# Performance work log

Hardware: AMD Instinct MI355X
Metric: run time of the kernel (lower is better)

## Reference

```python
import jax, jax.numpy as jnp
import numpy as np

E = 1024   # embed_dim
H = 16     # num_heads
DH = E // H
FF = 4096  # intermediate_size
EPS = 1e-5


def layernorm(x, g, b):
    mu = jnp.mean(x, axis=-1, keepdims=True)
    var = jnp.var(x, axis=-1, keepdims=True)
    return (x - mu) * jax.lax.rsqrt(var + EPS) * g + b


def setup_inputs() -> dict:
    key = jax.random.key(0)
    ks = jax.random.split(key, 16)
    s = 0.02
    return {
        "x": jax.random.normal(ks[0], (2, 2048, E), dtype=jnp.float32),
        "ln1_g": jnp.ones((E,), jnp.float32),
        "ln1_b": jnp.zeros((E,), jnp.float32),
        "ln2_g": jnp.ones((E,), jnp.float32),
        "ln2_b": jnp.zeros((E,), jnp.float32),
        # per-head Q/K/V projections stacked: [H, E, DH]
        "wq": jax.random.normal(ks[1], (H, E, DH), jnp.float32) * s,
        "bq": jnp.zeros((H, DH), jnp.float32),
        "wk": jax.random.normal(ks[2], (H, E, DH), jnp.float32) * s,
        "bk": jnp.zeros((H, DH), jnp.float32),
        "wv": jax.random.normal(ks[3], (H, E, DH), jnp.float32) * s,
        "bv": jnp.zeros((H, DH), jnp.float32),
        "wo": jax.random.normal(ks[4], (E, E), jnp.float32) * s,
        "bo": jnp.zeros((E,), jnp.float32),
        "w1": jax.random.normal(ks[5], (E, FF), jnp.float32) * s,
        "b1": jnp.zeros((FF,), jnp.float32),
        "w2": jax.random.normal(ks[6], (FF, E), jnp.float32) * s,
        "b2": jnp.zeros((E,), jnp.float32),
    }


def reference(x, ln1_g, ln1_b, ln2_g, ln2_b, wq, bq, wk, bk, wv, bv,
              wo, bo, w1, b1, w2, b2):
    # --- multi-head attention (pre-LN) ---
    h = layernorm(x, ln1_g, ln1_b)                       # [B,S,E]
    q = jnp.einsum('bse,hed->bhsd', h, wq) + bq[:, None, :]
    k = jnp.einsum('bse,hed->bhsd', h, wk) + bk[:, None, :]
    v = jnp.einsum('bse,hed->bhsd', h, wv) + bv[:, None, :]
    scores = jnp.einsum('bhsd,bhtd->bhst', q, k) / jnp.sqrt(
        jnp.asarray(DH, x.dtype))                        # [B,H,S,S]
    w = jax.nn.softmax(scores, axis=-1)
    attn = jnp.einsum('bhst,bhtd->bhsd', w, v)           # [B,H,S,DH]
    B, _, S, _ = attn.shape
    concat = attn.transpose(0, 2, 1, 3).reshape(B, S, E)  # head concat order
    x = x + concat @ wo + bo
    # --- feed-forward (pre-LN), exact GELU, dropout_p=0 ---
    h2 = layernorm(x, ln2_g, ln2_b)
    ff = jax.nn.gelu(h2 @ w1 + b1, approximate=False) @ w2 + b2
    return x + ff
```

## Files before the change

kernel.cpp:

```cpp
#include <hip/hip_runtime.h>
#include <hip/hip_bf16.h>
#include <math.h>

typedef __attribute__((ext_vector_type(8))) short short8;
typedef __attribute__((ext_vector_type(4))) float f32x4;
typedef __attribute__((ext_vector_type(16))) float f32x16;
typedef __attribute__((ext_vector_type(4))) unsigned u32x4;

#define MFMA_BF16(a, b, c) __builtin_amdgcn_mfma_f32_16x16x32_bf16(a, b, c, 0, 0, 0)
#define MFMA32_BF16(a, b, c) __builtin_amdgcn_mfma_f32_32x32x16_bf16(a, b, c, 0, 0, 0)
#define BAR() __builtin_amdgcn_s_barrier()

#define GLD_LDS16(g, l)                                              \
  __builtin_amdgcn_global_load_lds(                                  \
      (const __attribute__((address_space(1))) void*)(g),            \
      (__attribute__((address_space(3))) void*)(l), 16, 0, 0)

template <int N>
__device__ __forceinline__ void waitcnt_vm() {
  if constexpr (N == 0) asm volatile("s_waitcnt vmcnt(0)" ::: "memory");
  else if constexpr (N == 2) asm volatile("s_waitcnt vmcnt(2)" ::: "memory");
  else if constexpr (N == 4) asm volatile("s_waitcnt vmcnt(4)" ::: "memory");
  else if constexpr (N == 6) asm volatile("s_waitcnt vmcnt(6)" ::: "memory");
  else if constexpr (N == 8) asm volatile("s_waitcnt vmcnt(8)" ::: "memory");
}

__device__ __forceinline__ unsigned cvt_pk_bf16(float lo, float hi) {
  unsigned r;
  asm("v_cvt_pk_bf16_f32 %0, %1, %2" : "=v"(r) : "v"(lo), "v"(hi));
  return r;
}
#define PSWAP(a, b) asm volatile("v_permlane32_swap_b32 %0, %1" : "+v"(a), "+v"(b))

__device__ __forceinline__ unsigned short f2bf(float f) {
  union { float f; unsigned u; } v; v.f = f;
  unsigned r = v.u + 0x7FFFu + ((v.u >> 16) & 1u);
  return (unsigned short)(r >> 16);
}
__device__ __forceinline__ float bf2f(unsigned short u) {
  union { unsigned u; float f; } v; v.u = ((unsigned)u) << 16;
  return v.f;
}

__global__ __launch_bounds__(256) void transpose_cast(
    const float* __restrict__ in, unsigned short* __restrict__ out,
    int R, int C, size_t in_bs, size_t out_bs) {
  __shared__ float t[32][33];
  const float* inp = in + blockIdx.z * in_bs;
  unsigned short* outp = out + blockIdx.z * out_bs;
  const int c0 = blockIdx.x * 32, r0 = blockIdx.y * 32;
  const int tx = threadIdx.x, ty = threadIdx.y;
#pragma unroll
  for (int i = 0; i < 32; i += 8)
    t[ty + i][tx] = inp[(size_t)(r0 + ty + i) * C + c0 + tx];
  __syncthreads();
#pragma unroll
  for (int i = 0; i < 32; i += 8)
    outp[(size_t)(c0 + ty + i) * R + r0 + tx] = f2bf(t[tx][ty + i]);
}

__global__ void concat_bias(const float* __restrict__ bq, const float* __restrict__ bk,
                            const float* __restrict__ bv, float* __restrict__ bcat) {
  int i = blockIdx.x * 256 + threadIdx.x;
  if (i < 1024) bcat[i] = bq[i];
  else if (i < 2048) bcat[i] = bk[i - 1024];
  else if (i < 3072) bcat[i] = bv[i - 2048];
}

__global__ __launch_bounds__(512) void vtrans(
    const unsigned short* __restrict__ qkv, unsigned short* __restrict__ vt) {
  __shared__ unsigned short t[64][65];
  const int bh = blockIdx.y;
  const int s0 = blockIdx.x * 64;
  const int tx = threadIdx.x;
  const int ty = threadIdx.y;
  const unsigned short* in =
      qkv + (size_t)(bh >> 4) * 2048 * 3072 + 2048 + (bh & 15) * 64;
#pragma unroll
  for (int i = 0; i < 8; ++i)
    t[ty * 8 + i][tx] = in[(size_t)(s0 + ty * 8 + i) * 3072 + tx];
  __syncthreads();
  unsigned short* o = vt + (size_t)bh * 64 * 2048 + s0;
#pragma unroll
  for (int i = 0; i < 8; ++i)
    o[(size_t)(ty * 8 + i) * 2048 + tx] = t[tx][ty * 8 + i];
}

__global__ __launch_bounds__(256) void ln_kernel(
    const float* __restrict__ x, const float* __restrict__ g,
    const float* __restrict__ bb, unsigned short* __restrict__ out) {
  const int row = blockIdx.x, tid = threadIdx.x;
  const float4 v = ((const float4*)(x + (size_t)row * 1024))[tid];
  float s = v.x + v.y + v.z + v.w;
  float ss = v.x * v.x + v.y * v.y + v.z * v.z + v.w * v.w;
#pragma unroll
  for (int k = 1; k < 64; k <<= 1) {
    s += __shfl_xor(s, k, 64);
    ss += __shfl_xor(ss, k, 64);
  }
  __shared__ float red[8];
  const int wid = tid >> 6;
  if ((tid & 63) == 0) { red[wid] = s; red[wid + 4] = ss; }
  __syncthreads();
  s = red[0] + red[1] + red[2] + red[3];
  ss = red[4] + red[5] + red[6] + red[7];
  const float mu = s * (1.0f / 1024.0f);
  const float var = ss * (1.0f / 1024.0f) - mu * mu;
  const float rs = rsqrtf(var + 1e-5f);
  const float4 gv = ((const float4*)g)[tid];
  const float4 bv = ((const float4*)bb)[tid];
  ushort4 o;
  o.x = f2bf((v.x - mu) * rs * gv.x + bv.x);
  o.y = f2bf((v.y - mu) * rs * gv.y + bv.y);
  o.z = f2bf((v.z - mu) * rs * gv.z + bv.z);
  o.w = f2bf((v.w - mu) * rs * gv.w + bv.w);
  ((ushort4*)(out + (size_t)row * 1024))[tid] = o;
}

template <int QM, int QN>
__device__ __forceinline__ void mfq(f32x4 (&acc)[8][4], short8 (&af)[4][2],
                                    short8 (&bf)[2][2]) {
  __builtin_amdgcn_s_setprio(1);
#pragma unroll
  for (int i = 0; i < 4; ++i)
#pragma unroll
    for (int nf = 0; nf < 2; ++nf) {
      acc[QM * 4 + i][QN * 2 + nf] =
          MFMA_BF16(af[i][0], bf[nf][0], acc[QM * 4 + i][QN * 2 + nf]);
      acc[QM * 4 + i][QN * 2 + nf] =
          MFMA_BF16(af[i][1], bf[nf][1], acc[QM * 4 + i][QN * 2 + nf]);
    }
  __builtin_amdgcn_s_setprio(0);
}

template <int EPI>
__global__ __launch_bounds__(512, 2) void gemm256(
    const unsigned short* __restrict__ A, const unsigned short* __restrict__ Bt,
    const float* __restrict__ bias, void* __restrict__ Cout,
    int M, int N, int K,
    unsigned short* __restrict__ p0, unsigned short* __restrict__ p1,
    unsigned short* __restrict__ p2, unsigned short* __restrict__ p3) {
  extern __shared__ unsigned short L[];
  const int tid = threadIdx.x;
  const int wv = tid >> 6, lane = tid & 63;
  const int li = lane & 15, gi = lane >> 4;
  const int wm = wv >> 2, wn = wv & 3;
  const int bm = blockIdx.y, bn = blockIdx.x;
  const size_t Ksz = (size_t)K;
  const int KTloc = (K / (int)gridDim.z) >> 6;
  const int k0 = blockIdx.z * (KTloc << 6);

  auto lds = [&](int buf, int op, int half) -> unsigned short* {
    return L + (size_t)(((buf * 2 + op) * 2 + half)) * 8192;
  };

  const int sr8 = tid >> 3;
  const int segG = (tid & 7) ^ (sr8 & 7);
  const unsigned short* Ag = A + (size_t)(bm * 256 + sr8) * Ksz + segG * 8 + k0;
  const unsigned short* Bg = Bt + (size_t)(bn * 256 + sr8) * Ksz + segG * 8 + k0;
  const int wbase = wv * 512;

  auto stg = [&](int buf, int op, int half, int tile) {
    const unsigned short* g =
        (op ? Bg : Ag) + (size_t)(half * 128) * Ksz + (tile % KTloc) * 64;
    unsigned short* d = lds(buf, op, half);
    GLD_LDS16(g, d + wbase);
    GLD_LDS16(g + (size_t)64 * Ksz, d + 4096 + wbase);
  };

  f32x4 acc[8][4];
#pragma unroll
  for (int m = 0; m < 8; ++m)
#pragma unroll
    for (int n = 0; n < 4; ++n) acc[m][n] = (f32x4)0.0f;

  short8 af[4][2], b0[2][2], b1[2][2];
  auto ldA = [&](int buf, int qm) {
    const unsigned short* p = lds(buf, 0, wm);
#pragma unroll
    for (int i = 0; i < 4; ++i) {
      const int r = qm * 64 + i * 16 + li;
#pragma unroll
      for (int kk = 0; kk < 2; ++kk)
        af[i][kk] = *(const short8*)(p + r * 64 + (((kk * 4 + gi) ^ (r & 7)) * 8));
    }
  };
  auto ldB = [&](short8 (&bf)[2][2], int buf, int qn) {
    const unsigned short* p = lds(buf, 1, wn >> 1);
#pragma unroll
    for (int nf = 0; nf < 2; ++nf) {
      const int r = (wn & 1) * 64 + qn * 32 + nf * 16 + li;
#pragma unroll
      for (int kk = 0; kk < 2; ++kk)
        bf[nf][kk] = *(const short8*)(p + r * 64 + (((kk * 4 + gi) ^ (r & 7)) * 8));
    }
  };

  stg(0, 0, 0, 0); stg(0, 0, 1, 0); stg(0, 1, 0, 0); stg(0, 1, 1, 0);
  stg(1, 0, 0, 1);

  for (int j = 0; j < KTloc / 2; ++j) {
    const int t1 = 2 * j + 1, t2 = 2 * j + 2, t3 = 2 * j + 3;
    waitcnt_vm<2>(); BAR();
    ldA(0, 0); ldB(b0, 0, 0);
    stg(1, 0, 1, t1); stg(1, 1, 0, t1);
    BAR(); mfq<0, 0>(acc, af, b0); BAR();
    ldB(b1, 0, 1);
    stg(1, 1, 1, t1);
    BAR(); mfq<0, 1>(acc, af, b1); BAR();
    ldA(0, 1);
    stg(0, 0, 0, t2);
    BAR(); mfq<1, 0>(acc, af, b0); BAR();
    mfq<1, 1>(acc, af, b1); BAR();
    waitcnt_vm<2>(); BAR();
    ldA(1, 0); ldB(b0, 1, 0);
    stg(0, 0, 1, t2); stg(0, 1, 0, t2);
    BAR(); mfq<0, 0>(acc, af, b0); BAR();
    ldB(b1, 1, 1);
    stg(0, 1, 1, t2);
    BAR(); mfq<0, 1>(acc, af, b1); BAR();
    ldA(1, 1);
    stg(1, 0, 0, t3);
    BAR(); mfq<1, 0>(acc, af, b0); BAR();
    mfq<1, 1>(acc, af, b1); BAR();
  }

  unsigned short* Pz =
      (EPI == 3) ? ((blockIdx.z == 0) ? p0 : (blockIdx.z == 1) ? p1
                    : (blockIdx.z == 2) ? p2 : p3)
                 : (unsigned short*)Cout;
  const int row0 = bm * 256 + wm * 128 + gi * 4;
  const int col0 = bn * 256 + wn * 64 + li;
#pragma unroll
  for (int mf = 0; mf < 8; ++mf) {
#pragma unroll
    for (int nf = 0; nf < 4; ++nf) {
      const int col = col0 + nf * 16;
      const float bi = (EPI == 3) ? 0.0f : bias[col];
#pragma unroll
      for (int r = 0; r < 4; ++r) {
        const int row = row0 + mf * 16 + r;
        float v = acc[mf][nf][r] + bi;
        if (EPI == 2) v = 0.5f * v * (1.0f + erff(v * 0.70710678118654752f));
        Pz[(size_t)row * N + col] = f2bf(v);
      }
    }
  }
}

__global__ __launch_bounds__(256) void ffn2_combine(
    const unsigned short* __restrict__ p0, const unsigned short* __restrict__ p1,
    const unsigned short* __restrict__ p2, const unsigned short* __restrict__ p3,
    const float* __restrict__ b2, float* __restrict__ out) {
  const size_t i8 = (size_t)blockIdx.x * 256 + threadIdx.x;
  const size_t e0 = i8 * 8;
  const int col = (int)(e0 & 1023);
  const short8 a0 = *(const short8*)(p0 + e0);
  const short8 a1 = *(const short8*)(p1 + e0);
  const short8 a2 = *(const short8*)(p2 + e0);
  const short8 a3 = *(const short8*)(p3 + e0);
  float4 o0 = ((float4*)out)[i8 * 2];
  float4 o1 = ((float4*)out)[i8 * 2 + 1];
  float v[8];
#pragma unroll
  for (int j = 0; j < 8; ++j)
    v[j] = bf2f((unsigned short)a0[j]) + bf2f((unsigned short)a1[j]) +
           bf2f((unsigned short)a2[j]) + bf2f((unsigned short)a3[j]) + b2[col + j];
  o0.x += v[0]; o0.y += v[1]; o0.z += v[2]; o0.w += v[3];
  o1.x += v[4]; o1.y += v[5]; o1.z += v[6]; o1.w += v[7];
  ((float4*)out)[i8 * 2] = o0;
  ((float4*)out)[i8 * 2 + 1] = o1;
}

template <int EPI, int BN>
__global__ __launch_bounds__(256, (BN == 128) ? 2 : 3) void gemm_bt(
    const unsigned short* __restrict__ A, const unsigned short* __restrict__ Bt,
    const float* __restrict__ bias, const float* __restrict__ res,
    void* __restrict__ Cout, int M, int N, int K) {
  constexpr int NFR = BN / 32;
  constexpr int BISS = BN / 32;
  constexpr int ISS = 4 + BISS;
  __shared__ unsigned short As[2][128 * 64];
  __shared__ unsigned short Bs[2][BN * 64];
  const int tid = threadIdx.x;
  const int wid = tid >> 6, lane = tid & 63;
  const int li = lane & 15, gi = lane >> 4;
  const int bm = blockIdx.y, bn = blockIdx.x;
  const int wr = (wid >> 1) << 6;
  const int wc = (wid & 1) * (BN / 2);

  f32x4 acc[4][NFR];
#pragma unroll
  for (int m = 0; m < 4; ++m)
#pragma unroll
    for (int n = 0; n < NFR; ++n) acc[m][n] = (f32x4)0.0f;

  const size_t Ksz = (size_t)K;
  const int srow = tid >> 3;
  const int segG = (tid & 7) ^ (srow & 7);
  const unsigned short* Ab = A + (size_t)(bm * 128 + srow) * Ksz + segG * 8;
  const unsigned short* Bb = Bt + (size_t)(bn * BN + srow) * Ksz + segG * 8;

  auto stage = [&](int buf, int kt) {
#pragma unroll
    for (int c = 0; c < 4; ++c)
      GLD_LDS16(Ab + (size_t)(c * 32) * Ksz + kt, &As[buf][c * 2048 + wid * 512]);
#pragma unroll
    for (int c = 0; c < BISS; ++c)
      GLD_LDS16(Bb + (size_t)(c * 32) * Ksz + kt, &Bs[buf][c * 2048 + wid * 512]);
  };

  auto compute = [&](int ib) {
    const unsigned short* As_ = As[ib];
    const unsigned short* Bs_ = Bs[ib];
    short8 af[4][2], bf[NFR][2];
#pragma unroll
    for (int m = 0; m < 4; ++m)
#pragma unroll
      for (int kk = 0; kk < 2; ++kk) {
        const int row = wr + m * 16 + li;
        af[m][kk] = *(const short8*)(As_ + row * 64 + ((kk * 4 + gi) ^ (row & 7)) * 8);
      }
#pragma unroll
    for (int n = 0; n < NFR; ++n)
#pragma unroll
      for (int kk = 0; kk < 2; ++kk) {
        const int row = wc + n * 16 + li;
        bf[n][kk] = *(const short8*)(Bs_ + row * 64 + ((kk * 4 + gi) ^ (row & 7)) * 8);
      }
    __builtin_amdgcn_s_setprio(1);
#pragma unroll
    for (int m = 0; m < 4; ++m)
#pragma unroll
      for (int n = 0; n < NFR; ++n) {
        acc[m][n] = MFMA_BF16(af[m][0], bf[n][0], acc[m][n]);
        acc[m][n] = MFMA_BF16(af[m][1], bf[n][1], acc[m][n]);
      }
    __builtin_amdgcn_s_setprio(0);
  };

  const int KT = K >> 6;
  stage(0, 0);
  for (int i = 0; i < KT - 1; ++i) {
    stage((i + 1) & 1, (i + 1) << 6);
    waitcnt_vm<ISS>();
    __builtin_amdgcn_s_barrier();
    __builtin_amdgcn_sched_barrier(0);
    compute(i & 1);
    __builtin_amdgcn_s_barrier();
  }
  waitcnt_vm<0>();
  __builtin_amdgcn_s_barrier();
  __builtin_amdgcn_sched_barrier(0);
  compute((KT - 1) & 1);

  const int row_base = bm * 128 + wr + gi * 4;
  const int col_base = bn * BN + wc + li;
#pragma unroll
  for (int m = 0; m < 4; ++m) {
#pragma unroll
    for (int n = 0; n < NFR; ++n) {
      const int col = col_base + n * 16;
      const float bi = bias[col];
#pragma unroll
      for (int r = 0; r < 4; ++r) {
        const int row = row_base + m * 16 + r;
        float v = acc[m][n][r] + bi;
        if (EPI == 2) v = 0.5f * v * (1.0f + erff(v * 0.70710678118654752f));
        const size_t idx = (size_t)row * N + col;
        if (EPI == 1) ((float*)Cout)[idx] = v + res[idx];
        else ((unsigned short*)Cout)[idx] = f2bf(v);
      }
    }
  }
}

__global__ __launch_bounds__(256, 4) void attn_kernel(
    const unsigned short* __restrict__ qkv, const unsigned short* __restrict__ vt,
    unsigned short* __restrict__ op0, unsigned short* __restrict__ op1,
    float* __restrict__ lpart) {
  __shared__ unsigned short Kl[2][4096];
  __shared__ unsigned short Vl[2][4096];
  const int tid = threadIdx.x;
  const int wid = tid >> 6, lane = tid & 63;
  const int l31 = lane & 31, hiq = lane >> 5;
  const int kvh = blockIdx.z & 1, b = blockIdx.z >> 1, h = blockIdx.y;
  const int q0 = blockIdx.x * 128 + wid * 32;
  const int LD = 3072;
  const size_t base = (size_t)b * 2048 * LD;
  const size_t kvoff = (size_t)kvh * 1024 * LD;

  short8 qb[4];
  {
    const unsigned short* qp = qkv + base + (size_t)(q0 + l31) * LD + h * 64 + hiq * 8;
#pragma unroll
    for (int ds = 0; ds < 4; ++ds) qb[ds] = *(const short8*)(qp + ds * 16);
  }

  f32x16 o0 = (f32x16)0.0f, o1 = (f32x16)0.0f;
  float la = 0.0f, lb = 0.0f;

  const int rw = lane >> 3;
  const int sgG = (lane & 7) ^ rw;
  const unsigned short* kdma = qkv + base + kvoff + 1024 + h * 64 + sgG * 8 +
                               (size_t)(wid * 16 + rw) * LD;
  const unsigned short* vdma = vt + (size_t)(b * 16 + h) * 64 * 2048 +
                               (size_t)(wid * 16 + rw) * 2048 + kvh * 1024 + sgG * 8;

  auto kstage = [&](int buf, int t) {
    GLD_LDS16(kdma + (size_t)t * 64 * LD, &Kl[buf][wid * 1024]);
    GLD_LDS16(kdma + (size_t)(t * 64 + 8) * LD, &Kl[buf][wid * 1024 + 512]);
  };
  auto vstage = [&](int buf, int t) {
    GLD_LDS16(vdma + t * 64, &Vl[buf][wid * 1024]);
    GLD_LDS16(vdma + 8 * 2048 + t * 64, &Vl[buf][wid * 1024 + 512]);
  };

  auto compute = [&](int ib) {
    const unsigned short* kl = Kl[ib];
    const unsigned short* vl = Vl[ib];
    short8 kf[2][4];
#pragma unroll
    for (int kvb = 0; kvb < 2; ++kvb)
#pragma unroll
      for (int ds = 0; ds < 4; ++ds)
        kf[kvb][ds] = *(const short8*)(
            kl + (kvb * 32 + l31) * 64 + (((2 * ds + hiq) ^ (l31 & 7)) * 8));

    f32x16 sA = (f32x16)0.0f, sB = (f32x16)0.0f;
    __builtin_amdgcn_s_setprio(1);
#pragma unroll
    for (int ds = 0; ds < 4; ++ds) {
      sA = MFMA32_BF16(kf[0][ds], qb[ds], sA);
      sB = MFMA32_BF16(kf[1][ds], qb[ds], sB);
    }
    __builtin_amdgcn_s_setprio(0);

#pragma unroll
    for (int kvb = 0; kvb < 2; ++kvb) {
      const f32x16 s = kvb ? sB : sA;
      unsigned P[8];
#pragma unroll
      for (int i = 0; i < 8; ++i) {
        const float pe = __expf(s[2 * i] * 0.125f);
        const float po = __expf(s[2 * i + 1] * 0.125f);
        la += pe; lb += po;
        P[i] = cvt_pk_bf16(pe, po);
      }
      PSWAP(P[0], P[2]); PSWAP(P[1], P[3]);
      PSWAP(P[4], P[6]); PSWAP(P[5], P[7]);
      const short8 pa0 = __builtin_bit_cast(short8, (u32x4){P[0], P[1], P[2], P[3]});
      const short8 pa1 = __builtin_bit_cast(short8, (u32x4){P[4], P[5], P[6], P[7]});
      const int sg0 = 4 * kvb + hiq, sg1 = 4 * kvb + 2 + hiq;
      const short8 v00 = *(const short8*)(vl + l31 * 64 + ((sg0 ^ (l31 & 7)) * 8));
      const short8 v01 = *(const short8*)(vl + l31 * 64 + ((sg1 ^ (l31 & 7)) * 8));
      const short8 v10 = *(const short8*)(vl + (32 + l31) * 64 + ((sg0 ^ (l31 & 7)) * 8));
      const short8 v11 = *(const short8*)(vl + (32 + l31) * 64 + ((sg1 ^ (l31 & 7)) * 8));
      __builtin_amdgcn_s_setprio(1);
      o0 = MFMA32_BF16(pa0, v00, o0);
      o0 = MFMA32_BF16(pa1, v01, o0);
      o1 = MFMA32_BF16(pa0, v10, o1);
      o1 = MFMA32_BF16(pa1, v11, o1);
      __builtin_amdgcn_s_setprio(0);
    }
  };

  kstage(0, 0);
  vstage(0, 0);
  for (int t = 0; t < 15; ++t) {
    kstage((t + 1) & 1, t + 1);
    vstage((t + 1) & 1, t + 1);
    waitcnt_vm<4>();
    __builtin_amdgcn_s_barrier();
    __builtin_amdgcn_sched_barrier(0);
    compute(t & 1);
    __builtin_amdgcn_s_barrier();
  }
  waitcnt_vm<0>();
  __builtin_amdgcn_s_barrier();
  __builtin_amdgcn_sched_barrier(0);
  compute(15 & 1);

  const float lsum = la + lb;
  const float lt = lsum + __shfl_xor(lsum, 32, 64);
  if (hiq == 0)
    lpart[(size_t)kvh * 65536 + ((size_t)(b * 2048 + q0 + l31) * 16) + h] = lt;

  unsigned short* op = kvh ? op1 : op0;
#pragma unroll
  for (int r = 0; r < 16; ++r) {
    const int crow = (r & 3) + 8 * (r >> 2) + 4 * hiq;
    const size_t rowb = (size_t)(b * 2048 + q0 + crow) * 1024 + h * 64 + l31;
    op[rowb]      = f2bf(o0[r]);
    op[rowb + 32] = f2bf(o1[r]);
  }
}

__global__ __launch_bounds__(256) void attn_combine(
    const unsigned short* __restrict__ op0, unsigned short* __restrict__ op1io,
    const float* __restrict__ lpart) {
  const size_t i8 = (size_t)blockIdx.x * 256 + threadIdx.x;
  const size_t g = (i8 * 8) >> 6;
  const float inv = 1.0f / (lpart[g] + lpart[g + 65536]);
  const short8 a = *(const short8*)(op0 + i8 * 8);
  const short8 c = *(const short8*)(op1io + i8 * 8);
  short8 o;
#pragma unroll
  for (int j = 0; j < 8; ++j)
    o[j] = (short)f2bf((bf2f((unsigned short)a[j]) + bf2f((unsigned short)c[j])) * inv);
  *(short8*)(op1io + i8 * 8) = o;
}

extern "C" void kernel_launch(void* const* d_in, const int* in_sizes, int n_in,
                              void* d_out, int out_size, void* d_ws, size_t ws_size,
                              hipStream_t stream) {
  const float* x     = (const float*)d_in[0];
  const float* ln1_g = (const float*)d_in[1];
  const float* ln1_b = (const float*)d_in[2];
  const float* ln2_g = (const float*)d_in[3];
  const float* ln2_b = (const float*)d_in[4];
  const float* wq    = (const float*)d_in[5];
  const float* bq    = (const float*)d_in[6];
  const float* wk    = (const float*)d_in[7];
  const float* bk    = (const float*)d_in[8];
  const float* wv    = (const float*)d_in[9];
  const float* bv    = (const float*)d_in[10];
  const float* wo    = (const float*)d_in[11];
  const float* bo    = (const float*)d_in[12];
  const float* w1    = (const float*)d_in[13];
  const float* b1    = (const float*)d_in[14];
  const float* w2    = (const float*)d_in[15];
  const float* b2    = (const float*)d_in[16];
  float* out = (float*)d_out;

  hipFuncSetAttribute((const void*)gemm256<0>,
                      hipFuncAttributeMaxDynamicSharedMemorySize, 131072);
  hipFuncSetAttribute((const void*)gemm256<2>,
                      hipFuncAttributeMaxDynamicSharedMemorySize, 131072);
  hipFuncSetAttribute((const void*)gemm256<3>,
                      hipFuncAttributeMaxDynamicSharedMemorySize, 131072);

  char* p = (char*)d_ws;
  unsigned short* ws_h     = (unsigned short*)p; p += 4096ull * 1024 * 2;
  unsigned short* ws_qkv   = (unsigned short*)p; p += 4096ull * 3072 * 2;
  unsigned short* ws_attn  = (unsigned short*)p; p += 4096ull * 1024 * 2;
  unsigned short* ws_wqkvT = (unsigned short*)p; p += 3072ull * 1024 * 2;
  unsigned short* ws_woT   = (unsigned short*)p; p += 1024ull * 1024 * 2;
  unsigned short* ws_w1T   = (unsigned short*)p; p += 4096ull * 1024 * 2;
  unsigned short* ws_w2T   = (unsigned short*)p; p += 1024ull * 4096 * 2;
  float*          ws_bqkv  = (float*)p;          p += 3072 * 4;
  float*          ws_l     = (float*)p;          p += 2ull * 65536 * 4;
  unsigned short* ws_ff = ws_qkv;
  unsigned short* ws_vt = ws_w1T;
  unsigned short* ws_p0 = ws_h;
  unsigned short* ws_p1 = ws_attn;
  unsigned short* ws_p2 = ws_wqkvT;
  unsigned short* ws_p3 = ws_w1T;

  const dim3 tb(32, 8);
  transpose_cast<<<dim3(2, 32, 16), tb, 0, stream>>>(
      wq, ws_wqkvT, 1024, 64, (size_t)(1024 * 64), (size_t)(64 * 1024));
  transpose_cast<<<dim3(2, 32, 16), tb, 0, stream>>>(
      wk, ws_wqkvT + 1024ull * 1024, 1024, 64, (size_t)(1024 * 64), (size_t)(64 * 1024));
  transpose_cast<<<dim3(2, 32, 16), tb, 0, stream>>>(
      wv, ws_wqkvT + 2048ull * 1024, 1024, 64, (size_t)(1024 * 64), (size_t)(64 * 1024));
  transpose_cast<<<dim3(32, 32, 1), tb, 0, stream>>>(wo, ws_woT, 1024, 1024, 0, 0);
  concat_bias<<<12, 256, 0, stream>>>(bq, bk, bv, ws_bqkv);

  ln_kernel<<<4096, 256, 0, stream>>>(x, ln1_g, ln1_b, ws_h);
  gemm256<0><<<dim3(12, 16, 1), 512, 131072, stream>>>(
      ws_h, ws_wqkvT, ws_bqkv, ws_qkv, 4096, 3072, 1024,
      nullptr, nullptr, nullptr, nullptr);
  vtrans<<<dim3(32, 32), dim3(64, 8), 0, stream>>>(ws_qkv, ws_vt);
  attn_kernel<<<dim3(16, 16, 4), 256, 0, stream>>>(ws_qkv, ws_vt, ws_h, ws_attn, ws_l);
  attn_combine<<<2048, 256, 0, stream>>>(ws_h, ws_attn, ws_l);
  transpose_cast<<<dim3(128, 32, 1), tb, 0, stream>>>(w1, ws_w1T, 1024, 4096, 0, 0);
  transpose_cast<<<dim3(32, 128, 1), tb, 0, stream>>>(w2, ws_w2T, 4096, 1024, 0, 0);
  gemm_bt<1, 64><<<dim3(16, 32), 256, 0, stream>>>(ws_attn, ws_woT, bo, x,
                                                   out, 4096, 1024, 1024);
  ln_kernel<<<4096, 256, 0, stream>>>(out, ln2_g, ln2_b, ws_h);
  gemm256<2><<<dim3(16, 16, 1), 512, 131072, stream>>>(
      ws_h, ws_w1T, b1, ws_ff, 4096, 4096, 1024,
      nullptr, nullptr, nullptr, nullptr);
  gemm256<3><<<dim3(4, 16, 4), 512, 131072, stream>>>(
      ws_ff, ws_w2T, nullptr, nullptr, 4096, 1024, 4096,
      ws_p0, ws_p1, ws_p2, ws_p3);
  ffn2_combine<<<2048, 256, 0, stream>>>(ws_p0, ws_p1, ws_p2, ws_p3, b2, out);
}
```

Before: 244.3 us.

## Swizzle block order, hardcode K loop, and restructure GEMM/attention pipelines

The GEMM kernel remaps flat block indices with a stride-8 swizzle to improve L2 reuse. It hardcodes the K range per z-slice to 1024 (16 tiles), and reorders the staging, LDS loads and barriers so MFMA runs between fewer barriers. The attention kernel remaps blocks so neighbouring workgroups cover related heads and query tiles. Its loop now uses one barrier per iteration, issuing the next K/V prefetch after the barrier instead of before the wait. The hardcoded K=1024 per split assumes specific launch shapes, and the single-barrier scheme depends on the new ordering to avoid LDS races.

```diff
diff --git a/kernel.cpp b/kernel.cpp
--- a/kernel.cpp
+++ b/kernel.cpp
@@ -138,17 +138,19 @@
     const unsigned short* __restrict__ A, const unsigned short* __restrict__ Bt,
     const float* __restrict__ bias, void* __restrict__ Cout,
     int M, int N, int K,
-    unsigned short* __restrict__ p0, unsigned short* __restrict__ p1,
-    unsigned short* __restrict__ p2, unsigned short* __restrict__ p3) {
+    unsigned short* __restrict__ p0p, unsigned short* __restrict__ p1p,
+    unsigned short* __restrict__ p2p, unsigned short* __restrict__ p3p) {
   extern __shared__ unsigned short L[];
   const int tid = threadIdx.x;
   const int wv = tid >> 6, lane = tid & 63;
   const int li = lane & 15, gi = lane >> 4;
   const int wm = wv >> 2, wn = wv & 3;
-  const int bm = blockIdx.y, bn = blockIdx.x;
+  const int gx = gridDim.x;
+  const int flat = blockIdx.y * gx + blockIdx.x;
+  const int swz = (flat & 7) * ((gx * gridDim.y) >> 3) + (flat >> 3);
+  const int bm = swz / gx, bn = swz - bm * gx;
   const size_t Ksz = (size_t)K;
-  const int KTloc = (K / (int)gridDim.z) >> 6;
-  const int k0 = blockIdx.z * (KTloc << 6);
+  const int k0 = (int)(blockIdx.z << 10);
 
   auto lds = [&](int buf, int op, int half) -> unsigned short* {
     return L + (size_t)(((buf * 2 + op) * 2 + half)) * 8192;
@@ -162,7 +164,7 @@
 
   auto stg = [&](int buf, int op, int half, int tile) {
     const unsigned short* g =
-        (op ? Bg : Ag) + (size_t)(half * 128) * Ksz + (tile % KTloc) * 64;
+        (op ? Bg : Ag) + (size_t)(half * 128) * Ksz + (tile & 15) * 64;
     unsigned short* d = lds(buf, op, half);
     GLD_LDS16(g, d + wbase);
     GLD_LDS16(g + (size_t)64 * Ksz, d + 4096 + wbase);
@@ -199,35 +201,43 @@
   stg(0, 0, 0, 0); stg(0, 0, 1, 0); stg(0, 1, 0, 0); stg(0, 1, 1, 0);
   stg(1, 0, 0, 1);
 
-  for (int j = 0; j < KTloc / 2; ++j) {
+  for (int j = 0; j < 8; ++j) {
     const int t1 = 2 * j + 1, t2 = 2 * j + 2, t3 = 2 * j + 3;
-    waitcnt_vm<2>(); BAR();
+    waitcnt_vm<2>();
+    BAR();
+    stg(1, 0, 1, t1); stg(1, 1, 0, t1);
     ldA(0, 0); ldB(b0, 0, 0);
-    stg(1, 0, 1, t1); stg(1, 1, 0, t1);
-    BAR(); mfq<0, 0>(acc, af, b0); BAR();
+    mfq<0, 0>(acc, af, b0);
+    BAR();
+    stg(1, 1, 1, t1);
     ldB(b1, 0, 1);
-    stg(1, 1, 1, t1);
-    BAR(); mfq<0, 1>(acc, af, b1); BAR();
+    mfq<0, 1>(acc, af, b1);
+    BAR();
     ldA(0, 1);
+    mfq<1, 0>(acc, af, b0);
+    BAR();
     stg(0, 0, 0, t2);
-    BAR(); mfq<1, 0>(acc, af, b0); BAR();
-    mfq<1, 1>(acc, af, b1); BAR();
-    waitcnt_vm<2>(); BAR();
+    mfq<1, 1>(acc, af, b1);
+    waitcnt_vm<2>();
+    BAR();
+    stg(0, 0, 1, t2); stg(0, 1, 0, t2);
     ldA(1, 0); ldB(b0, 1, 0);
-    stg(0, 0, 1, t2); stg(0, 1, 0, t2);
-    BAR(); mfq<0, 0>(acc, af, b0); BAR();
+    mfq<0, 0>(acc, af, b0);
+    BAR();
+    stg(0, 1, 1, t2);
     ldB(b1, 1, 1);
-    stg(0, 1, 1, t2);
-    BAR(); mfq<0, 1>(acc, af, b1); BAR();
+    mfq<0, 1>(acc, af, b1);
+    BAR();
     ldA(1, 1);
+    mfq<1, 0>(acc, af, b0);
+    BAR();
     stg(1, 0, 0, t3);
-    BAR(); mfq<1, 0>(acc, af, b0); BAR();
-    mfq<1, 1>(acc, af, b1); BAR();
+    mfq<1, 1>(acc, af, b1);
   }
 
   unsigned short* Pz =
-      (EPI == 3) ? ((blockIdx.z == 0) ? p0 : (blockIdx.z == 1) ? p1
-                    : (blockIdx.z == 2) ? p2 : p3)
+      (EPI == 3) ? ((blockIdx.z == 0) ? p0p : (blockIdx.z == 1) ? p1p
+                    : (blockIdx.z == 2) ? p2p : p3p)
                  : (unsigned short*)Cout;
   const int row0 = bm * 256 + wm * 128 + gi * 4;
   const int col0 = bn * 256 + wn * 64 + li;
@@ -384,8 +394,10 @@
   const int tid = threadIdx.x;
   const int wid = tid >> 6, lane = tid & 63;
   const int l31 = lane & 31, hiq = lane >> 5;
-  const int kvh = blockIdx.z & 1, b = blockIdx.z >> 1, h = blockIdx.y;
-  const int q0 = blockIdx.x * 128 + wid * 32;
+  const int kvh = blockIdx.z & 1, b = blockIdx.z >> 1;
+  const int g = blockIdx.y * 16 + blockIdx.x;
+  const int h = (g & 7) * 2 + (g >> 7);
+  const int q0 = ((g >> 3) & 15) * 128 + wid * 32;
   const int LD = 3072;
   const size_t base = (size_t)b * 2048 * LD;
   const size_t kvoff = (size_t)kvh * 1024 * LD;
@@ -467,19 +479,12 @@
 
   kstage(0, 0);
   vstage(0, 0);
-  for (int t = 0; t < 15; ++t) {
-    kstage((t + 1) & 1, t + 1);
-    vstage((t + 1) & 1, t + 1);
-    waitcnt_vm<4>();
+  for (int t = 0; t < 16; ++t) {
+    waitcnt_vm<0>();
     __builtin_amdgcn_s_barrier();
-    __builtin_amdgcn_sched_barrier(0);
+    if (t < 15) { kstage((t + 1) & 1, t + 1); vstage((t + 1) & 1, t + 1); }
     compute(t & 1);
-    __builtin_amdgcn_s_barrier();
-  }
-  waitcnt_vm<0>();
-  __builtin_amdgcn_s_barrier();
-  __builtin_amdgcn_sched_barrier(0);
-  compute(15 & 1);
+  }
 
   const float lsum = la + lb;
   const float lt = lsum + __shfl_xor(lsum, 32, 64);
```

Result: faster. 237.1 us (-3.0%).
